# Kernel tuning notes

Measured on AMD Instinct MI355X. Metric: run time of the kernel, lower is better.

## Reference

```python
import jax, jax.numpy as jnp
import numpy as np
import math

F = 32; NB = 8; MAXZ = 55; CUTOFF = 5.0; NIT = 3
B = 32; N = 32

def _cgc(j1, m1, j2, m2, J, M):
    if m1 + m2 != M or J < abs(j1 - j2) or J > j1 + j2: return 0.0
    f = math.factorial
    pref = (2*J+1)*f(J+j1-j2)*f(J-j1+j2)*f(j1+j2-J)/f(j1+j2+J+1)
    pref *= f(J+M)*f(J-M)*f(j1-m1)*f(j1+m1)*f(j2-m2)*f(j2+m2)
    s = 0.0
    for k in range(0, j1+j2+1):
        d = [j1+j2-J-k, j1-m1-k, j2+m2-k, J-j2+m1+k, J-j1-m2+k]
        if any(x < 0 for x in d): continue
        s += (-1)**k/(f(k)*f(d[0])*f(d[1])*f(d[2])*f(d[3])*f(d[4]))
    return math.sqrt(pref)*s

def _U(l):
    M = np.zeros((2*l+1, 2*l+1), dtype=np.complex128); M[l, l] = 1.0
    for m in range(1, l+1):
        M[l+m, l+m] = (-1)**m/math.sqrt(2); M[l+m, l-m] = 1/math.sqrt(2)
        M[l-m, l-m] = 1j/math.sqrt(2); M[l-m, l+m] = -1j*(-1)**m/math.sqrt(2)
    return M

def _build_cg():
    cg = np.zeros((9, 9, 9), dtype=np.float64)
    for l1 in range(3):
        for l2 in range(3):
            for l3 in range(3):
                if l3 < abs(l1-l2) or l3 > l1+l2: continue
                C = np.zeros((2*l1+1, 2*l2+1, 2*l3+1))
                for a, m1 in enumerate(range(-l1, l1+1)):
                    for b, m2 in enumerate(range(-l2, l2+1)):
                        for c, m3 in enumerate(range(-l3, l3+1)):
                            C[a, b, c] = _cgc(l1, m1, l2, m2, l3, m3)
                G = np.einsum('am,bn,co,mno->abc', _U(l1), _U(l2), np.conj(_U(l3)), C.astype(np.complex128))
                R = np.where(np.abs(G.imag) > np.abs(G.real), G.imag, G.real)
                cg[l1*l1:(l1+1)**2, l2*l2:(l2+1)**2, l3*l3:(l3+1)**2] = R
    return cg.astype(np.float32)

CG = jnp.asarray(_build_cg())
DM = np.array([0, 1, 1, 1, 2, 2, 2, 2, 2])
EVEN_B = jnp.asarray((DM % 2 == 0).astype(np.float32))
ODD_B = jnp.asarray((DM % 2 == 1).astype(np.float32))

def _degmask(maxdeg):
    return jnp.asarray((DM <= maxdeg).astype(np.float32))

def _sph(u):
    x, y, z = u[..., 0], u[..., 1], u[..., 2]
    s3 = math.sqrt(3.0)
    return jnp.stack([jnp.ones_like(x), y, z, x, s3*x*y, s3*y*z, 0.5*(3*z*z - 1.0), s3*x*z, 0.5*s3*(x*x - y*y)], axis=-1)

def _radial(r):
    f = 1.0/(1.0 + r)
    k = jnp.arange(NB, dtype=f.dtype)
    binom = jnp.asarray([math.comb(NB-1, i) for i in range(NB)], dtype=jnp.float32)
    rb = binom*(f[:, None]**k)*((1.0 - f[:, None])**(NB-1-k))
    u2 = (r/CUTOFF)**2
    cut = jnp.where(r < CUTOFF, jnp.exp(1.0 - 1.0/jnp.clip(1.0 - u2, 1e-6, None)), 0.0)
    return rb*cut[:, None]

def _dense(x, W, b):
    y = jnp.einsum('npmf,fg->npmg', x, W)
    return y.at[:, 0, 0, :].add(b)

def _silu(x):
    return x*jax.nn.sigmoid(x[:, :1, :1, :])

def _expand_path(Wp):  # (3,3,3,F) -> (9,9,9,F) by degree of each m index
    return Wp[DM[:, None, None], DM[None, :, None], DM[None, None, :]]

def _couple(x1, x2, Wp, maxdeg):
    cgw = CG[..., None]*_expand_path(Wp)
    def cp(a, b):
        return jnp.einsum('nabf,abcf->ncf', jnp.einsum('naf,nbf->nabf', a, b), cgw)
    p0 = cp(x1[:, 0], x2[:, 0]) + cp(x1[:, 1], x2[:, 1])
    p1 = cp(x1[:, 0], x2[:, 1]) + cp(x1[:, 1], x2[:, 0])
    return jnp.stack([p0, p1], axis=1)*_degmask(maxdeg)[None, None, :, None]

def _tensor_dense(x, W1, W2, Wp, maxdeg):
    u = jnp.einsum('npmf,fg->npmg', x, W1)
    v = jnp.einsum('npmf,fg->npmg', x, W2)
    return _couple(u, v, Wp, maxdeg)

def _message_pass(x, sh, rad, Wmp, dst, src, nseg, maxdeg):
    # g[e,b,f] = Y_b(r_hat_e) * (radial_e @ Wmp[deg(b)])
    g = sh[:, :, None]*jnp.einsum('en,bnf->ebf', rad, Wmp[DM])
    ge = g*EVEN_B[None, :, None]; go = g*ODD_B[None, :, None]
    xs = x[src]
    def cp(a, b):
        return jnp.einsum('eabf,abc->ecf', jnp.einsum('eaf,ebf->eabf', a, b), CG)
    y0 = cp(xs[:, 0], ge) + cp(xs[:, 1], go)
    y1 = cp(xs[:, 0], go) + cp(xs[:, 1], ge)
    msg = jnp.stack([y0, y1], axis=1)*_degmask(maxdeg)[None, None, :, None]
    return jax.ops.segment_sum(msg, dst, num_segments=nseg)

def _forward(atomic_numbers, positions, Ef, dst_idx, src_idx, batch_size,
             embed, Wmp, Wd, bd, Wt, Wtd1, Wtd2, Wtdp, Wh, bh, Wq,
             Wdip1, Wdip2, Wdipp, wdip, We, be, element_bias):
    Z = atomic_numbers.reshape(-1)
    pos = positions.reshape(-1, 3)
    Bv = int(batch_size); BNv = Z.shape[0]; Nn = BNv // Bv
    offsets = (jnp.arange(Bv, dtype=dst_idx.dtype)*Nn)
    dst = (dst_idx[None, :] + offsets[:, None]).reshape(-1)
    src = (src_idx[None, :] + offsets[:, None]).reshape(-1)
    batch_segments = jnp.repeat(jnp.arange(Bv, dtype=jnp.int32), Nn)
    disp = pos[src] - pos[dst]
    r = jnp.linalg.norm(disp, axis=-1)
    u = disp/(r[:, None] + 1e-10)
    sh = _sph(u); rad = _radial(r)
    # external field features: vector Ef in the degree-1 slots (m = 1..3)
    ef_rep = jnp.repeat(Ef, Nn, axis=0)
    xEF = jnp.zeros((BNv, 2, 9, F), dtype=pos.dtype).at[:, :, 1:4, :].set(ef_rep[:, None, :, None])
    # atomic-number embedding lives in the even scalar channel
    x = jnp.zeros((BNv, 2, 9, F), dtype=pos.dtype).at[:, 0, 0, :].set(embed[Z])
    for i in range(NIT):
        md = 2 if i < NIT - 1 else 0
        y = _message_pass(x, sh, rad, Wmp[i], dst, src, BNv, md)
        x = x + y
        x = _silu(x)
        x = _dense(x, Wd[i], bd[i])
        x = _silu(x)
        xEF = _couple(x, xEF, Wt[i], 2)
        x = x + xEF
        x = _tensor_dense(x, Wtd1[i], Wtd2[i], Wtdp[i], 2)
        x = x + y
    for i in range(4):
        x = _silu(_dense(x, Wh[i], bh[i]))
    x = _dense(x, Wh[4], bh[4])
    x_orig = x
    scal = x[:, 0, 0, :]
    charges = scal @ Wq
    # dipole head: proper tensors up to degree 1 -> TensorDense -> vector readout
    xd = jnp.zeros_like(x_orig)
    xd = xd.at[:, 0, 0, :].set(x_orig[:, 0, 0, :])
    xd = xd.at[:, 1, 1:4, :].set(x_orig[:, 1, 1:4, :])
    xd = _tensor_dense(xd, Wdip1, Wdip2, Wdipp, 1)
    atomic_dipoles = jnp.einsum('ncf,f->nc', xd[:, 1, 1:4, :], wdip)
    pos_b = pos.reshape(Bv, Nn, 3)
    q_b = charges.reshape(Bv, Nn)
    d_b = atomic_dipoles.reshape(Bv, Nn, 3)
    com = pos_b.mean(axis=1, keepdims=True)
    dipole = jnp.sum(q_b[:, :, None]*(pos_b - com), axis=1) + d_b.sum(axis=1)
    aE = scal @ We + be + element_bias[Z]
    energy = aE.reshape(Bv, Nn).sum(axis=1)
    pair = charges[src]*charges[dst]/(r + 1e-10)
    coul = jax.ops.segment_sum(pair, batch_segments[dst], num_segments=Bv)/2.0
    energy = energy + coul*14.399645
    return energy, dipole

def setup_inputs() -> dict:
    key = jax.random.key(0)
    ks = jax.random.split(key, 20)
    pos = jax.random.uniform(ks[0], (B, N, 3), dtype=jnp.float32)*8.0
    Z = jax.random.randint(ks[1], (B, N), 1, MAXZ + 1)
    Ef = jax.random.normal(ks[2], (B, 3), dtype=jnp.float32)*0.01
    ii, jj = np.meshgrid(np.arange(N), np.arange(N), indexing='ij')
    mask = ii != jj
    dst_idx = jnp.asarray(ii[mask].astype(np.int32))
    src_idx = jnp.asarray(jj[mask].astype(np.int32))
    s = 1.0/math.sqrt(F)
    def nrm(k, shape, sc=s):
        return jax.random.normal(k, shape, dtype=jnp.float32)*sc
    return {
        'atomic_numbers': Z, 'positions': pos, 'Ef': Ef,
        'dst_idx': dst_idx, 'src_idx': src_idx, 'batch_size': B,
        'embed': nrm(ks[3], (MAXZ + 1, F), 1.0),
        'Wmp': nrm(ks[4], (NIT, 3, NB, F)),
        'Wd': nrm(ks[5], (NIT, F, F)), 'bd': jnp.zeros((NIT, F), jnp.float32),
        'Wt': nrm(ks[6], (NIT, 3, 3, 3, F)),
        'Wtd1': nrm(ks[7], (NIT, F, F)), 'Wtd2': nrm(ks[8], (NIT, F, F)),
        'Wtdp': nrm(ks[9], (NIT, 3, 3, 3, F)),
        'Wh': nrm(ks[10], (5, F, F)), 'bh': jnp.zeros((5, F), jnp.float32),
        'Wq': nrm(ks[11], (F,), 0.1*s),
        'Wdip1': nrm(ks[12], (F, F)), 'Wdip2': nrm(ks[13], (F, F)),
        'Wdipp': nrm(ks[14], (3, 3, 3, F)), 'wdip': nrm(ks[15], (F,), 0.1*s),
        'We': nrm(ks[16], (F,), 0.1*s), 'be': jnp.zeros((), jnp.float32),
        'element_bias': nrm(ks[17], (MAXZ + 1,), 0.1),
    }

def reference(atomic_numbers, positions, Ef, dst_idx, src_idx, batch_size,
              embed, Wmp, Wd, bd, Wt, Wtd1, Wtd2, Wtdp, Wh, bh, Wq,
              Wdip1, Wdip2, Wdipp, wdip, We, be, element_bias):
    return _forward(atomic_numbers, positions, Ef, dst_idx, src_idx, batch_size,
                    embed, Wmp, Wd, bd, Wt, Wtd1, Wtd2, Wtdp, Wh, bh, Wq,
                    Wdip1, Wdip2, Wdipp, wdip, We, be, element_bias)
```

## Files before the change

### kernel.cpp

```cpp
#include <hip/hip_runtime.h>
#include <utility>
#include <type_traits>


namespace cgb {
constexpr double SQ2 = 1.4142135623730951;
constexpr double cabs_(double x){ return x < 0 ? -x : x; }
constexpr double fact(int n){ double r = 1.0; for (int i = 2; i <= n; ++i) r *= (double)i; return r; }
constexpr double csqrt(double x){
  if (x <= 0.0) return 0.0;
  double g = x > 1.0 ? x : 1.0;
  for (int i = 0; i < 48; ++i) g = 0.5 * (g + x / g);
  return g;
}
constexpr double cgc(int j1,int m1,int j2,int m2,int J,int M){
  if (m1 + m2 != M) return 0.0;
  int ad = j1 - j2; if (ad < 0) ad = -ad;
  if (J < ad || J > j1 + j2) return 0.0;
  double pref = (2.0*J+1.0) * fact(J+j1-j2) * fact(J-j1+j2) * fact(j1+j2-J) / fact(j1+j2+J+1);
  pref *= fact(J+M)*fact(J-M)*fact(j1-m1)*fact(j1+m1)*fact(j2-m2)*fact(j2+m2);
  double s = 0.0;
  for (int k = 0; k <= j1+j2; ++k){
    int d0=j1+j2-J-k, d1=j1-m1-k, d2=j2+m2-k, d3=J-j2+m1+k, d4=J-j1-m2+k;
    if (d0<0||d1<0||d2<0||d3<0||d4<0) continue;
    double t = 1.0/(fact(k)*fact(d0)*fact(d1)*fact(d2)*fact(d3)*fact(d4));
    s += (k & 1) ? -t : t;
  }
  return csqrt(pref) * s;
}
struct C2 { double re, im; };
struct URow { int n; int col[2]; C2 v[2]; };
constexpr URow urow(int l, int r){
  URow u{};
  if (r == l){ u.n = 1; u.col[0] = l; u.v[0] = C2{1.0, 0.0}; return u; }
  if (r > l){
    int m = r - l; double sg = (m & 1) ? -1.0 : 1.0;
    u.n = 2;
    u.col[0] = l + m; u.v[0] = C2{ sg / SQ2, 0.0 };
    u.col[1] = l - m; u.v[1] = C2{ 1.0 / SQ2, 0.0 };
    return u;
  }
  int m = l - r; double sg = (m & 1) ? -1.0 : 1.0;
  u.n = 2;
  u.col[0] = l - m; u.v[0] = C2{ 0.0, 1.0 / SQ2 };
  u.col[1] = l + m; u.v[1] = C2{ 0.0, -sg / SQ2 };
  return u;
}
struct Tab { float v[9][9][9]; };
constexpr Tab build(){
  Tab t{};
  for (int l1 = 0; l1 < 3; ++l1)
  for (int l2 = 0; l2 < 3; ++l2)
  for (int l3 = 0; l3 < 3; ++l3){
    int ad = l1 - l2; if (ad < 0) ad = -ad;
    if (l3 < ad || l3 > l1 + l2) continue;
    double C[5][5][5] = {};
    for (int m = 0; m < 2*l1+1; ++m)
      for (int n = 0; n < 2*l2+1; ++n){
        int o = (m - l1) + (n - l2) + l3;
        if (o < 0 || o > 2*l3) continue;
        C[m][n][o] = cgc(l1, m-l1, l2, n-l2, l3, o-l3);
      }
    for (int a = 0; a < 2*l1+1; ++a)
    for (int b = 0; b < 2*l2+1; ++b)
    for (int c = 0; c < 2*l3+1; ++c){
      URow ua = urow(l1,a), ub = urow(l2,b), uc = urow(l3,c);
      double gre = 0.0, gim = 0.0;
      for (int i = 0; i < ua.n; ++i)
      for (int j = 0; j < ub.n; ++j)
      for (int k = 0; k < uc.n; ++k){
        double Cv = C[ua.col[i]][ub.col[j]][uc.col[k]];
        if (Cv == 0.0) continue;
        double r1 = ua.v[i].re*ub.v[j].re - ua.v[i].im*ub.v[j].im;
        double i1 = ua.v[i].re*ub.v[j].im + ua.v[i].im*ub.v[j].re;
        double cr = uc.v[k].re, ci = -uc.v[k].im;
        gre += (r1*cr - i1*ci) * Cv;
        gim += (r1*ci + i1*cr) * Cv;
      }
      double r = (cabs_(gim) > cabs_(gre)) ? gim : gre;
      t.v[l1*l1+a][l2*l2+b][l3*l3+c] = (float)r;
    }
  }
  return t;
}
constexpr Tab CGT = build();
}

constexpr int DM_[9] = {0,1,1,1,2,2,2,2,2};

template<class F, int... Is>
__device__ __forceinline__ void sf_impl(F&& f, std::integer_sequence<int, Is...>){
  (f(std::integral_constant<int, Is>{}), ...);
}
template<int N, class F>
__device__ __forceinline__ void static_for(F&& f){
  sf_impl(static_cast<F&&>(f), std::make_integer_sequence<int, N>{});
}

__device__ __forceinline__ float rsum32(float v){
  #pragma unroll
  for (int s = 16; s > 0; s >>= 1) v += __shfl_xor(v, s, 32);
  return v;
}

__device__ __forceinline__ float dot32_lds(const float* sm, int xrow_off,
                                           const float (&wcol)[32]){
  float acc = 0.f;
  #pragma unroll
  for (int i = 0; i < 8; ++i){
    float4 xv = *reinterpret_cast<const float4*>(&sm[xrow_off + 4*i]);
    acc = fmaf(xv.x, wcol[4*i+0], acc);
    acc = fmaf(xv.y, wcol[4*i+1], acc);
    acc = fmaf(xv.z, wcol[4*i+2], acc);
    acc = fmaf(xv.w, wcol[4*i+3], acc);
  }
  return acc;
}

__device__ __forceinline__ void dense_hg(float* sm, int xoff,
                                         const float* __restrict__ W,
                                         int ooff, int f, int hg){
  float wcol[32];
  #pragma unroll
  for (int fp = 0; fp < 32; ++fp) wcol[fp] = W[fp*32 + f];
  for (int m = hg; m < 18; m += 8)
    sm[ooff + m*32 + f] = dot32_lds(sm, xoff + m*32, wcol);
}

__device__ __forceinline__ void dense_silu_hg(float* sm, int xoff,
                                              const float* __restrict__ W,
                                              const float* __restrict__ bias,
                                              int ooff, int f, int hg){
  float wcol[32];
  #pragma unroll
  for (int fp = 0; fp < 32; ++fp) wcol[fp] = W[fp*32 + f];
  float acc0 = dot32_lds(sm, xoff, wcol);
  float b = bias[f];
  float gate = 1.f / (1.f + expf(-(acc0 + b)));
  for (int m = hg; m < 18; m += 8){
    float acc = (m == 0) ? (acc0 + b) : dot32_lds(sm, xoff + m*32, wcol);
    sm[ooff + m*32 + f] = acc * gate;
  }
}

template<int OUTMODE>
__device__ __forceinline__ void couple_stage(float* sm, int x1o, int x2o,
                                             const float* __restrict__ Wp,
                                             int dsto, int addo,
                                             float* gout, float* gef,
                                             int f, int wv, int q){
  int r2a = x2o + q*9*32 + f;
  int r2b = x2o + (q^1)*9*32 + f;
  static_for<9>([&](auto C){
    constexpr int c = C.value;
    if ((c & 3) == wv){
      bool need = true;
      if constexpr (OUTMODE == 3) need = q ? (c >= 1 && c <= 3) : (c == 0);
      if (need){
        float out = 0.f;
        static_for<81>([&](auto AB){
          constexpr int a = AB.value / 9, b = AB.value % 9;
          constexpr float v = cgb::CGT.v[a][b][c];
          if constexpr (v != 0.0f){
            constexpr int path = (DM_[a]*3 + DM_[b])*3 + DM_[c];
            float w   = v * Wp[path*32 + f];
            float x10 = sm[x1o + a*32 + f];
            float x11 = sm[x1o + (9+a)*32 + f];
            out = fmaf(w, fmaf(x10, sm[r2a + b*32], x11*sm[r2b + b*32]), out);
          }
        });
        int row = (q*9 + c)*32 + f;
        if constexpr (OUTMODE == 0){
          sm[dsto + row] = out + sm[addo + row];
          if (gef) gef[row] = out;
        }
        if constexpr (OUTMODE == 1) gout[row] = out + sm[addo + row];
        if constexpr (OUTMODE == 3){
          int slot = q ? c : 0;
          sm[dsto + slot*32 + f] = out + sm[addo + row];
        }
      }
    }
  });
}

#define L_WL   0
#define L_GEO  768
#define L_XB   1360
#define L_EB   1936
#define L_YB   2512
#define L_RED  3088
#define L_TOT  5392
#define L_HA   (L_RED)
#define L_HB   (L_RED + 128)
#define L_TU   (L_RED + 256)
#define L_TV   (L_RED + 384)

struct KParams {
  const float* POS; const int* Z; const float* Ef;
  const int* src;
  const float* embed;
  const float* Wmp; const float* Wd; const float* bd;
  const float* Wt; const float* Wtd1; const float* Wtd2; const float* Wtdp;
  const float* Wh; const float* bh; const float* Wq;
  const float* Wdip1; const float* Wdip2; const float* Wdipp; const float* wdip;
  const float* We; const float* be; const float* ebias;
  const float* Xc; float* Xn; float* XEF;
  float* Q; float* AE; float* AD;
};

template<int MODE>
__global__ __launch_bounds__(256) void k_iter(KParams p){
  __shared__ __align__(16) float sm[L_TOT];
  int tid = threadIdx.x;
  int f = tid & 31, hg = tid >> 5, wv = tid >> 6, q = (tid >> 5) & 1;
  int n = ((blockIdx.x & 7) << 7) | (blockIdx.x >> 3);
  int bi = n >> 5, d = n & 31;

  if (tid < 31){
    int t = tid;
    int s = bi*32 + p.src[d*31 + t];
    float dx = p.POS[s*3+0] - p.POS[n*3+0];
    float dy = p.POS[s*3+1] - p.POS[n*3+1];
    float dz = p.POS[s*3+2] - p.POS[n*3+2];
    float r  = sqrtf(dx*dx + dy*dy + dz*dz);
    float inv = 1.0f / (r + 1e-10f);
    float x = dx*inv, y = dy*inv, z = dz*inv;
    const float s3 = 1.7320508075688772f;
    float* gp = &sm[L_GEO + t*19];
    gp[0] = 1.0f; gp[1] = y; gp[2] = z; gp[3] = x;
    gp[4] = s3*x*y; gp[5] = s3*y*z; gp[6] = 0.5f*(3.0f*z*z - 1.0f);
    gp[7] = s3*x*z; gp[8] = 0.5f*s3*(x*x - y*y);
    float fr = 1.0f / (1.0f + r);
    float om = 1.0f - fr;
    float frk[8]; frk[0] = 1.0f;
    #pragma unroll
    for (int kk = 1; kk < 8; ++kk) frk[kk] = frk[kk-1]*fr;
    float omk[8]; omk[0] = 1.0f;
    #pragma unroll
    for (int kk = 1; kk < 8; ++kk) omk[kk] = omk[kk-1]*om;
    const float bin[8] = {1.f,7.f,21.f,35.f,35.f,21.f,7.f,1.f};
    float u2 = (r*0.2f)*(r*0.2f);
    float cut = 0.0f;
    if (r < 5.0f){
      float den = fmaxf(1.0f - u2, 1e-6f);
      cut = expf(1.0f - 1.0f/den);
    }
    #pragma unroll
    for (int kk = 0; kk < 8; ++kk) gp[9+kk] = bin[kk]*frk[kk]*omk[7-kk]*cut;
    gp[18] = __int_as_float(s);
  } else if (tid >= 32){
    int t2 = tid - 32;
    for (int j = t2; j < 768; j += 224) sm[L_WL+j] = p.Wmp[j];
    if constexpr (MODE == 0){
      float e3[3] = { p.Ef[bi*3+0], p.Ef[bi*3+1], p.Ef[bi*3+2] };
      for (int j2 = t2; j2 < 576; j2 += 224){
        int m = (j2 >> 5) % 9;
        sm[L_EB + j2] = (m >= 1 && m <= 3) ? e3[m-1] : 0.f;
      }
    } else {
      const float* erow = p.XEF + (size_t)n*576;
      for (int j2 = t2; j2 < 576; j2 += 224) sm[L_EB+j2] = erow[j2];
    }
  }
  __syncthreads();

  float acc[2][9];
  #pragma unroll
  for (int pp = 0; pp < 2; ++pp)
    #pragma unroll
    for (int c = 0; c < 9; ++c) acc[pp][c] = 0.0f;

  #pragma unroll
  for (int k = 0; k < 4; ++k){
    int t = hg + 8*k;
    if (t < 31){
      const float* gp = &sm[L_GEO + t*19];
      float wt0 = 0.f, wt1 = 0.f, wt2 = 0.f;
      #pragma unroll
      for (int nb = 0; nb < 8; ++nb){
        float rv = gp[9+nb];
        wt0 = fmaf(rv, sm[L_WL + (0*8+nb)*32 + f], wt0);
        wt1 = fmaf(rv, sm[L_WL + (1*8+nb)*32 + f], wt1);
        wt2 = fmaf(rv, sm[L_WL + (2*8+nb)*32 + f], wt2);
      }
      float g[9];
      g[0] = gp[0]*wt0;
      g[1] = gp[1]*wt1; g[2] = gp[2]*wt1; g[3] = gp[3]*wt1;
      g[4] = gp[4]*wt2; g[5] = gp[5]*wt2; g[6] = gp[6]*wt2;
      g[7] = gp[7]*wt2; g[8] = gp[8]*wt2;
      int s = __float_as_int(gp[18]);

      if constexpr (MODE == 0){
        float x00 = p.embed[p.Z[s]*32 + f];
        static_for<9>([&](auto C){
          constexpr int c = C.value;
          constexpr int pb = DM_[c] & 1;
          acc[pb][c] = fmaf(g[c], x00, acc[pb][c]);
        });
      } else {
        const float* xp = p.Xc + (size_t)s*576 + f;
        static_for<9>([&](auto A){
          constexpr int a = A.value;
          float x0a = xp[a*32];
          float x1a = xp[(9+a)*32];
          static_for<81>([&](auto BC){
            constexpr int b = BC.value / 9, c = BC.value % 9;
            constexpr float v = cgb::CGT.v[a][b][c];
            if constexpr (v != 0.0f){
              constexpr int pb = DM_[b] & 1;
              float tg = v * g[b];
              acc[0][c] = fmaf(tg, pb ? x1a : x0a, acc[0][c]);
              acc[1][c] = fmaf(tg, pb ? x0a : x1a, acc[1][c]);
            }
          });
        });
      }
    }
  }
  #pragma unroll
  for (int pp = 0; pp < 2; ++pp)
    #pragma unroll
    for (int c = 0; c < 9; ++c) acc[pp][c] += __shfl_xor(acc[pp][c], 32);
  if ((tid & 63) < 32){
    #pragma unroll
    for (int pp = 0; pp < 2; ++pp)
      #pragma unroll
      for (int c = 0; c < 9; ++c) sm[L_RED + wv*576 + (pp*9+c)*32 + f] = acc[pp][c];
  }
  __syncthreads();

  {
    const float* xrow = (MODE == 0) ? nullptr : (p.Xc + (size_t)n*576);
    int zn = 0;
    if constexpr (MODE == 0) zn = p.Z[n];
    for (int j2 = tid; j2 < 576; j2 += 256){
      int jm = (j2 >> 5) % 9;
      int ff = j2 & 31;
      float y = sm[L_RED+j2] + sm[L_RED+576+j2] + sm[L_RED+1152+j2] + sm[L_RED+1728+j2];
      if (MODE == 2 && jm != 0) y = 0.f;
      float y0 = sm[L_RED+ff] + sm[L_RED+576+ff] + sm[L_RED+1152+ff] + sm[L_RED+1728+ff];
      float xv, x0;
      if constexpr (MODE == 0){
        xv = (j2 < 32) ? p.embed[zn*32 + j2] : 0.f;
        x0 = p.embed[zn*32 + ff];
      } else {
        xv = xrow[j2];
        x0 = xrow[ff];
      }
      float gate = 1.f / (1.f + expf(-(x0 + y0)));
      sm[L_YB + j2] = y;
      sm[L_XB + j2] = (xv + y) * gate;
    }
  }
  __syncthreads();

  dense_silu_hg(sm, L_XB, p.Wd, p.bd, L_RED, f, hg);
  __syncthreads();

  {
    float* erow = (MODE < 2) ? (p.XEF + (size_t)n*576) : nullptr;
    couple_stage<0>(sm, L_RED, L_EB, p.Wt, L_XB, L_RED, nullptr, erow, f, wv, q);
  }
  __syncthreads();

  dense_hg(sm, L_XB, p.Wtd1, L_RED + 576,  f, hg);
  dense_hg(sm, L_XB, p.Wtd2, L_RED + 1152, f, hg);
  __syncthreads();

  if constexpr (MODE < 2){
    couple_stage<1>(sm, L_RED + 576, L_RED + 1152, p.Wtdp, 0, L_YB,
                    p.Xn + (size_t)n*576, nullptr, f, wv, q);
    return;
  } else {
    couple_stage<3>(sm, L_RED + 576, L_RED + 1152, p.Wtdp, L_HA, L_YB,
                    nullptr, nullptr, f, wv, q);
  }
  __syncthreads();

  #pragma unroll
  for (int k = 0; k < 5; ++k){
    int srco = (k & 1) ? L_HB : L_HA;
    int dsto = (k & 1) ? L_HA : L_HB;
    if (hg < 4){
      float wcol[32];
      #pragma unroll
      for (int fp = 0; fp < 32; ++fp) wcol[fp] = p.Wh[k*1024 + fp*32 + f];
      float acc0 = dot32_lds(sm, srco, wcol);
      float b = p.bh[k*32 + f];
      float accr = (hg == 0) ? acc0 : dot32_lds(sm, srco + hg*32, wcol);
      float val = accr + ((hg == 0) ? b : 0.f);
      if (k < 4) val *= 1.f / (1.f + expf(-(acc0 + b)));
      sm[dsto + hg*32 + f] = val;
    }
    __syncthreads();
  }

  {
    int mat = hg >> 2;
    int slot = hg & 3;
    const float* W = mat ? p.Wdip2 : p.Wdip1;
    float wcol[32];
    #pragma unroll
    for (int fp = 0; fp < 32; ++fp) wcol[fp] = W[fp*32 + f];
    float acc2 = dot32_lds(sm, L_HB + slot*32, wcol);
    sm[(mat ? L_TV : L_TU) + slot*32 + f] = acc2;
  }
  __syncthreads();

  if (tid < 32){
    float scal = sm[L_HB + f];
    float qv = rsum32(scal * p.Wq[f]);
    float ae = rsum32(scal * p.We[f]) + p.be[0] + p.ebias[p.Z[n]];
    float u00 = sm[L_TU + f], v00 = sm[L_TV + f];
    float wp4  = p.Wdipp[4*32 + f];
    float wp10 = p.Wdipp[10*32 + f];
    float wd = p.wdip[f];
    float ad[3];
    #pragma unroll
    for (int c = 1; c <= 3; ++c){
      float p1 = wp4*u00*sm[L_TV + c*32 + f] + wp10*sm[L_TU + c*32 + f]*v00;
      ad[c-1] = rsum32(p1 * wd);
    }
    if (f == 0){
      p.Q[n] = qv;
      p.AE[n] = ae;
      p.AD[3*n+0] = ad[0]; p.AD[3*n+1] = ad[1]; p.AD[3*n+2] = ad[2];
    }
  }
}

__global__ __launch_bounds__(64) void k_final(const float* __restrict__ Q,
                                              const float* __restrict__ AE,
                                              const float* __restrict__ AD,
                                              const float* __restrict__ POS,
                                              const int* __restrict__ dst_idx,
                                              const int* __restrict__ src_idx,
                                              float* __restrict__ out,
                                              int Nn, int Eb, int Bv){
  __shared__ float qs[32];
  __shared__ float ps[32][3];
  int b = blockIdx.x, tid = threadIdx.x;
  float q = 0.f, ae = 0.f, px = 0.f, py = 0.f, pz = 0.f, ax = 0.f, ay = 0.f, az = 0.f;
  if (tid < Nn){
    int n = b*Nn + tid;
    q  = Q[n]; ae = AE[n];
    px = POS[n*3+0]; py = POS[n*3+1]; pz = POS[n*3+2];
    ax = AD[3*n+0]; ay = AD[3*n+1]; az = AD[3*n+2];
    qs[tid] = q;
    ps[tid][0] = px; ps[tid][1] = py; ps[tid][2] = pz;
  }
  __syncthreads();
  float invN = 1.0f / (float)Nn;
  float cx = rsum32(px) * invN;
  float cy = rsum32(py) * invN;
  float cz = rsum32(pz) * invN;
  float dipx = rsum32(q*(px - cx) + ax);
  float dipy = rsum32(q*(py - cy) + ay);
  float dipz = rsum32(q*(pz - cz) + az);
  float sae  = rsum32(ae);

  float cl = 0.0f;
  for (int e = tid; e < Eb; e += 64){
    int dd = dst_idx[e], ss = src_idx[e];
    float dx = ps[ss][0] - ps[dd][0];
    float dy = ps[ss][1] - ps[dd][1];
    float dz = ps[ss][2] - ps[dd][2];
    float r = sqrtf(dx*dx + dy*dy + dz*dz);
    cl += qs[ss]*qs[dd] / (r + 1e-10f);
  }
  #pragma unroll
  for (int s = 32; s > 0; s >>= 1) cl += __shfl_xor(cl, s, 64);

  if (tid == 0){
    out[b] = sae + 0.5f*cl*14.399645f;
    out[Bv + b*3 + 0] = dipx;
    out[Bv + b*3 + 1] = dipy;
    out[Bv + b*3 + 2] = dipz;
  }
}

extern "C" void kernel_launch(void* const* d_in, const int* in_sizes, int n_in,
                              void* d_out, int out_size, void* d_ws, size_t ws_size,
                              hipStream_t stream) {
  (void)n_in; (void)out_size; (void)ws_size;
  const int*   Z     = (const int*)  d_in[0];
  const float* POS   = (const float*)d_in[1];
  const float* Ef    = (const float*)d_in[2];
  const int*   dst   = (const int*)  d_in[3];
  const int*   src   = (const int*)  d_in[4];
  const float* embed = (const float*)d_in[6];
  const float* Wmp   = (const float*)d_in[7];
  const float* Wd    = (const float*)d_in[8];
  const float* bd    = (const float*)d_in[9];
  const float* Wt    = (const float*)d_in[10];
  const float* Wtd1  = (const float*)d_in[11];
  const float* Wtd2  = (const float*)d_in[12];
  const float* Wtdp  = (const float*)d_in[13];
  const float* Wh    = (const float*)d_in[14];
  const float* bh    = (const float*)d_in[15];
  const float* Wq    = (const float*)d_in[16];
  const float* Wdip1 = (const float*)d_in[17];
  const float* Wdip2 = (const float*)d_in[18];
  const float* Wdipp = (const float*)d_in[19];
  const float* wdip  = (const float*)d_in[20];
  const float* We    = (const float*)d_in[21];
  const float* be    = (const float*)d_in[22];
  const float* ebias = (const float*)d_in[23];

  const int BN = in_sizes[0];
  const int Bv = in_sizes[2] / 3;
  const int Nn = BN / Bv;
  const int Eb = in_sizes[3];

  float* wsf = (float*)d_ws;
  float* Xa  = wsf;
  float* Xb  = Xa  + (size_t)BN*576;
  float* XEF = Xb  + (size_t)BN*576;
  float* Qb  = XEF + (size_t)BN*576;
  float* AEb = Qb  + BN;
  float* AD  = AEb + BN;

  KParams p{};
  p.POS = POS; p.Z = Z; p.Ef = Ef; p.src = src; p.embed = embed;
  p.Wh = Wh; p.bh = bh; p.Wq = Wq;
  p.Wdip1 = Wdip1; p.Wdip2 = Wdip2; p.Wdipp = Wdipp; p.wdip = wdip;
  p.We = We; p.be = be; p.ebias = ebias;
  p.Q = Qb; p.AE = AEb; p.AD = AD;

  p.Wmp = Wmp; p.Wd = Wd; p.bd = bd; p.Wt = Wt;
  p.Wtd1 = Wtd1; p.Wtd2 = Wtd2; p.Wtdp = Wtdp;
  p.Xc = Xa; p.Xn = Xa; p.XEF = XEF;
  k_iter<0><<<BN, 256, 0, stream>>>(p);

  p.Wmp = Wmp + 768; p.Wd = Wd + 1024; p.bd = bd + 32; p.Wt = Wt + 864;
  p.Wtd1 = Wtd1 + 1024; p.Wtd2 = Wtd2 + 1024; p.Wtdp = Wtdp + 864;
  p.Xc = Xa; p.Xn = Xb;
  k_iter<1><<<BN, 256, 0, stream>>>(p);

  p.Wmp = Wmp + 2*768; p.Wd = Wd + 2*1024; p.bd = bd + 2*32; p.Wt = Wt + 2*864;
  p.Wtd1 = Wtd1 + 2*1024; p.Wtd2 = Wtd2 + 2*1024; p.Wtdp = Wtdp + 2*864;
  p.Xc = Xb; p.Xn = Xa;
  k_iter<2><<<BN, 256, 0, stream>>>(p);

  k_final<<<Bv, 64, 0, stream>>>(Qb, AEb, AD, POS, dst, src,
                                 (float*)d_out, Nn, Eb, Bv);
}
```

Baseline: 85.23 us.

## Fuse final reduction into last iteration via last-block atomic counter

Removes the separate k_final launch. Each molecule's last-finishing block in the third iteration kernel performs the dipole and Coulomb reduction, chosen through an atomic per-molecule counter that is cleared by a memset. The readout MLP now runs on one wave with no block barriers, and the node-feature row is prefetched at kernel start to hide global latency. The memset adds a small launch, and sizes such as 32 molecules and 992 edges are now hardcoded.

```diff
diff --git a/kernel.cpp b/kernel.cpp
--- a/kernel.cpp
+++ b/kernel.cpp
@@ -195,10 +195,12 @@
 #define L_HB   (L_RED + 128)
 #define L_TU   (L_RED + 256)
 #define L_TV   (L_RED + 384)
+#define L_QS   (L_RED + 512)
+#define L_PS   (L_RED + 544)
 
 struct KParams {
   const float* POS; const int* Z; const float* Ef;
-  const int* src;
+  const int* src; const int* dst;
   const float* embed;
   const float* Wmp; const float* Wd; const float* bd;
   const float* Wt; const float* Wtd1; const float* Wtd2; const float* Wtdp;
@@ -207,6 +209,7 @@
   const float* We; const float* be; const float* ebias;
   const float* Xc; float* Xn; float* XEF;
   float* Q; float* AE; float* AD;
+  float* out; int* gcnt;
 };
 
 template<int MODE>
@@ -216,6 +219,15 @@
   int f = tid & 31, hg = tid >> 5, wv = tid >> 6, q = (tid >> 5) & 1;
   int n = ((blockIdx.x & 7) << 7) | (blockIdx.x >> 3);
   int bi = n >> 5, d = n & 31;
+
+  float xpre0 = 0.f, xpre1 = 0.f, xpre2 = 0.f, x0pre = 0.f;
+  if constexpr (MODE != 0){
+    const float* xrow = p.Xc + (size_t)n*576;
+    x0pre = xrow[f];
+    xpre0 = xrow[tid];
+    xpre1 = xrow[tid + 256];
+    if (tid < 64) xpre2 = xrow[tid + 512];
+  }
 
   if (tid < 31){
     int t = tid;
@@ -331,26 +343,27 @@
   __syncthreads();
 
   {
-    const float* xrow = (MODE == 0) ? nullptr : (p.Xc + (size_t)n*576);
     int zn = 0;
     if constexpr (MODE == 0) zn = p.Z[n];
-    for (int j2 = tid; j2 < 576; j2 += 256){
-      int jm = (j2 >> 5) % 9;
-      int ff = j2 & 31;
-      float y = sm[L_RED+j2] + sm[L_RED+576+j2] + sm[L_RED+1152+j2] + sm[L_RED+1728+j2];
-      if (MODE == 2 && jm != 0) y = 0.f;
-      float y0 = sm[L_RED+ff] + sm[L_RED+576+ff] + sm[L_RED+1152+ff] + sm[L_RED+1728+ff];
-      float xv, x0;
-      if constexpr (MODE == 0){
-        xv = (j2 < 32) ? p.embed[zn*32 + j2] : 0.f;
-        x0 = p.embed[zn*32 + ff];
-      } else {
-        xv = xrow[j2];
-        x0 = xrow[ff];
-      }
-      float gate = 1.f / (1.f + expf(-(x0 + y0)));
-      sm[L_YB + j2] = y;
-      sm[L_XB + j2] = (xv + y) * gate;
+    float y0 = sm[L_RED+f] + sm[L_RED+576+f] + sm[L_RED+1152+f] + sm[L_RED+1728+f];
+    float x0 = (MODE == 0) ? p.embed[zn*32 + f] : x0pre;
+    float gate = 1.f / (1.f + expf(-(x0 + y0)));
+    #pragma unroll
+    for (int jj = 0; jj < 3; ++jj){
+      int j2 = tid + jj*256;
+      if (jj < 2 || tid < 64){
+        int jm = (j2 >> 5) % 9;
+        float y = sm[L_RED+j2] + sm[L_RED+576+j2] + sm[L_RED+1152+j2] + sm[L_RED+1728+j2];
+        if (MODE == 2 && jm != 0) y = 0.f;
+        float xv;
+        if constexpr (MODE == 0){
+          xv = (j2 < 32) ? p.embed[zn*32 + j2] : 0.f;
+        } else {
+          xv = (jj == 0) ? xpre0 : (jj == 1) ? xpre1 : xpre2;
+        }
+        sm[L_YB + j2] = y;
+        sm[L_XB + j2] = (xv + y) * gate;
+      }
     }
   }
   __syncthreads();
@@ -378,36 +391,40 @@
   }
   __syncthreads();
 
+  if (tid >= 64) return;
+  int half = tid >> 5;
+
   #pragma unroll
   for (int k = 0; k < 5; ++k){
     int srco = (k & 1) ? L_HB : L_HA;
     int dsto = (k & 1) ? L_HA : L_HB;
-    if (hg < 4){
-      float wcol[32];
-      #pragma unroll
-      for (int fp = 0; fp < 32; ++fp) wcol[fp] = p.Wh[k*1024 + fp*32 + f];
-      float acc0 = dot32_lds(sm, srco, wcol);
-      float b = p.bh[k*32 + f];
-      float accr = (hg == 0) ? acc0 : dot32_lds(sm, srco + hg*32, wcol);
-      float val = accr + ((hg == 0) ? b : 0.f);
-      if (k < 4) val *= 1.f / (1.f + expf(-(acc0 + b)));
-      sm[dsto + hg*32 + f] = val;
-    }
-    __syncthreads();
+    float wcol[32];
+    #pragma unroll
+    for (int fp = 0; fp < 32; ++fp) wcol[fp] = p.Wh[k*1024 + fp*32 + f];
+    float acc0 = dot32_lds(sm, srco, wcol);
+    float b = p.bh[k*32 + f];
+    float gate = (k < 4) ? 1.f / (1.f + expf(-(acc0 + b))) : 1.f;
+    int r1 = 2*half, r2 = 2*half + 1;
+    float v1 = (r1 == 0) ? acc0 : dot32_lds(sm, srco + r1*32, wcol);
+    float v2 = dot32_lds(sm, srco + r2*32, wcol);
+    v1 += (r1 == 0) ? b : 0.f;
+    if (k < 4){ v1 *= gate; v2 *= gate; }
+    sm[dsto + r1*32 + f] = v1;
+    sm[dsto + r2*32 + f] = v2;
   }
 
   {
-    int mat = hg >> 2;
-    int slot = hg & 3;
-    const float* W = mat ? p.Wdip2 : p.Wdip1;
+    const float* W = half ? p.Wdip2 : p.Wdip1;
+    int ooff = half ? L_TV : L_TU;
     float wcol[32];
     #pragma unroll
     for (int fp = 0; fp < 32; ++fp) wcol[fp] = W[fp*32 + f];
-    float acc2 = dot32_lds(sm, L_HB + slot*32, wcol);
-    sm[(mat ? L_TV : L_TU) + slot*32 + f] = acc2;
-  }
-  __syncthreads();
-
+    #pragma unroll
+    for (int slot = 0; slot < 4; ++slot)
+      sm[ooff + slot*32 + f] = dot32_lds(sm, L_HB + slot*32, wcol);
+  }
+
+  int lastv = 0;
   if (tid < 32){
     float scal = sm[L_HB + f];
     float qv = rsum32(scal * p.Wq[f]);
@@ -423,60 +440,64 @@
       ad[c-1] = rsum32(p1 * wd);
     }
     if (f == 0){
-      p.Q[n] = qv;
-      p.AE[n] = ae;
-      p.AD[3*n+0] = ad[0]; p.AD[3*n+1] = ad[1]; p.AD[3*n+2] = ad[2];
-    }
-  }
-}
-
-__global__ __launch_bounds__(64) void k_final(const float* __restrict__ Q,
-                                              const float* __restrict__ AE,
-                                              const float* __restrict__ AD,
-                                              const float* __restrict__ POS,
-                                              const int* __restrict__ dst_idx,
-                                              const int* __restrict__ src_idx,
-                                              float* __restrict__ out,
-                                              int Nn, int Eb, int Bv){
-  __shared__ float qs[32];
-  __shared__ float ps[32][3];
-  int b = blockIdx.x, tid = threadIdx.x;
-  float q = 0.f, ae = 0.f, px = 0.f, py = 0.f, pz = 0.f, ax = 0.f, ay = 0.f, az = 0.f;
-  if (tid < Nn){
-    int n = b*Nn + tid;
-    q  = Q[n]; ae = AE[n];
-    px = POS[n*3+0]; py = POS[n*3+1]; pz = POS[n*3+2];
-    ax = AD[3*n+0]; ay = AD[3*n+1]; az = AD[3*n+2];
-    qs[tid] = q;
-    ps[tid][0] = px; ps[tid][1] = py; ps[tid][2] = pz;
-  }
-  __syncthreads();
-  float invN = 1.0f / (float)Nn;
-  float cx = rsum32(px) * invN;
-  float cy = rsum32(py) * invN;
-  float cz = rsum32(pz) * invN;
-  float dipx = rsum32(q*(px - cx) + ax);
-  float dipy = rsum32(q*(py - cy) + ay);
-  float dipz = rsum32(q*(pz - cz) + az);
-  float sae  = rsum32(ae);
-
+      __hip_atomic_store(&p.Q[n],  qv, __ATOMIC_RELAXED, __HIP_MEMORY_SCOPE_AGENT);
+      __hip_atomic_store(&p.AE[n], ae, __ATOMIC_RELAXED, __HIP_MEMORY_SCOPE_AGENT);
+      __hip_atomic_store(&p.AD[3*n+0], ad[0], __ATOMIC_RELAXED, __HIP_MEMORY_SCOPE_AGENT);
+      __hip_atomic_store(&p.AD[3*n+1], ad[1], __ATOMIC_RELAXED, __HIP_MEMORY_SCOPE_AGENT);
+      __hip_atomic_store(&p.AD[3*n+2], ad[2], __ATOMIC_RELAXED, __HIP_MEMORY_SCOPE_AGENT);
+      __threadfence();
+      int old = __hip_atomic_fetch_add(&p.gcnt[bi], 1, __ATOMIC_ACQ_REL,
+                                       __HIP_MEMORY_SCOPE_AGENT);
+      lastv = (old == 31) ? 1 : 0;
+    }
+  }
+  lastv = __shfl(lastv, 0, 64);
+  if (!lastv) return;
+  __threadfence();
+
+  float qv2 = 0.f, ae2 = 0.f, px = 0.f, py = 0.f, pz = 0.f;
+  float ax = 0.f, ay = 0.f, az = 0.f;
+  if (tid < 32){
+    int nn = bi*32 + tid;
+    qv2 = __hip_atomic_load(&p.Q[nn],  __ATOMIC_RELAXED, __HIP_MEMORY_SCOPE_AGENT);
+    ae2 = __hip_atomic_load(&p.AE[nn], __ATOMIC_RELAXED, __HIP_MEMORY_SCOPE_AGENT);
+    ax  = __hip_atomic_load(&p.AD[3*nn+0], __ATOMIC_RELAXED, __HIP_MEMORY_SCOPE_AGENT);
+    ay  = __hip_atomic_load(&p.AD[3*nn+1], __ATOMIC_RELAXED, __HIP_MEMORY_SCOPE_AGENT);
+    az  = __hip_atomic_load(&p.AD[3*nn+2], __ATOMIC_RELAXED, __HIP_MEMORY_SCOPE_AGENT);
+    px = p.POS[nn*3+0]; py = p.POS[nn*3+1]; pz = p.POS[nn*3+2];
+    sm[L_QS + tid] = qv2;
+    sm[L_PS + tid]      = px;
+    sm[L_PS + 32 + tid] = py;
+    sm[L_PS + 64 + tid] = pz;
+  }
+  float sae = 0.f, dipx = 0.f, dipy = 0.f, dipz = 0.f;
+  if (tid < 32){
+    const float invN = 1.0f / 32.0f;
+    float cx = rsum32(px) * invN;
+    float cy = rsum32(py) * invN;
+    float cz = rsum32(pz) * invN;
+    dipx = rsum32(qv2*(px - cx) + ax);
+    dipy = rsum32(qv2*(py - cy) + ay);
+    dipz = rsum32(qv2*(pz - cz) + az);
+    sae  = rsum32(ae2);
+  }
   float cl = 0.0f;
-  for (int e = tid; e < Eb; e += 64){
-    int dd = dst_idx[e], ss = src_idx[e];
-    float dx = ps[ss][0] - ps[dd][0];
-    float dy = ps[ss][1] - ps[dd][1];
-    float dz = ps[ss][2] - ps[dd][2];
+  for (int e = tid; e < 992; e += 64){
+    int dd = p.dst[e], ss = p.src[e];
+    float dx = sm[L_PS+ss] - sm[L_PS+dd];
+    float dy = sm[L_PS+32+ss] - sm[L_PS+32+dd];
+    float dz = sm[L_PS+64+ss] - sm[L_PS+64+dd];
     float r = sqrtf(dx*dx + dy*dy + dz*dz);
-    cl += qs[ss]*qs[dd] / (r + 1e-10f);
+    cl += sm[L_QS+ss]*sm[L_QS+dd] / (r + 1e-10f);
   }
   #pragma unroll
   for (int s = 32; s > 0; s >>= 1) cl += __shfl_xor(cl, s, 64);
 
   if (tid == 0){
-    out[b] = sae + 0.5f*cl*14.399645f;
-    out[Bv + b*3 + 0] = dipx;
-    out[Bv + b*3 + 1] = dipy;
-    out[Bv + b*3 + 2] = dipz;
+    p.out[bi] = sae + 0.5f*cl*14.399645f;
+    p.out[32 + bi*3 + 0] = dipx;
+    p.out[32 + bi*3 + 1] = dipy;
+    p.out[32 + bi*3 + 2] = dipz;
   }
 }
 
@@ -509,9 +530,6 @@
   const float* ebias = (const float*)d_in[23];
 
   const int BN = in_sizes[0];
-  const int Bv = in_sizes[2] / 3;
-  const int Nn = BN / Bv;
-  const int Eb = in_sizes[3];
 
   float* wsf = (float*)d_ws;
   float* Xa  = wsf;
@@ -520,13 +538,17 @@
   float* Qb  = XEF + (size_t)BN*576;
   float* AEb = Qb  + BN;
   float* AD  = AEb + BN;
+  int*   gcnt = (int*)(AD + 3*BN);
+
+  hipMemsetAsync((void*)gcnt, 0, 32*sizeof(int), stream);
 
   KParams p{};
-  p.POS = POS; p.Z = Z; p.Ef = Ef; p.src = src; p.embed = embed;
+  p.POS = POS; p.Z = Z; p.Ef = Ef; p.src = src; p.dst = dst; p.embed = embed;
   p.Wh = Wh; p.bh = bh; p.Wq = Wq;
   p.Wdip1 = Wdip1; p.Wdip2 = Wdip2; p.Wdipp = Wdipp; p.wdip = wdip;
   p.We = We; p.be = be; p.ebias = ebias;
   p.Q = Qb; p.AE = AEb; p.AD = AD;
+  p.out = (float*)d_out; p.gcnt = gcnt;
 
   p.Wmp = Wmp; p.Wd = Wd; p.bd = bd; p.Wt = Wt;
   p.Wtd1 = Wtd1; p.Wtd2 = Wtd2; p.Wtdp = Wtdp;
@@ -542,7 +564,4 @@
   p.Wtd1 = Wtd1 + 2*1024; p.Wtd2 = Wtd2 + 2*1024; p.Wtdp = Wtdp + 2*864;
   p.Xc = Xb; p.Xn = Xa;
   k_iter<2><<<BN, 256, 0, stream>>>(p);
-
-  k_final<<<Bv, 64, 0, stream>>>(Qb, AEb, AD, POS, dst, src,
-                                 (float*)d_out, Nn, Eb, Bv);
-}
+}
```

Measured after the change: 123.4 us. +44.8%, slower.
